# Optimization experiments

Measured on AMD Instinct MI355X. Metric: run time of the kernel, lower is better.

The kernel has to match this reference:

```python
import jax, jax.numpy as jnp
import numpy as np

L = 8          # number of QTT cores = log2(init_reso)
RESO = 256     # init_reso
MAX_RANK = 256
N_SAMPLES = 4096


def _qtt_ranks(L, max_rank):
    return [min(8 ** k, 8 ** (L - k), max_rank) for k in range(L + 1)]


def setup_inputs() -> dict:
    key = jax.random.key(0)
    ranks = _qtt_ranks(L, MAX_RANK)
    keys = jax.random.split(key, L + 1)
    inp = {}
    for l in range(L):
        shape = (ranks[l], 8, ranks[l + 1])
        scale = (shape[0] * shape[1]) ** -0.5  # keep chain products O(1)
        inp[f"core{l}"] = jax.random.normal(keys[l], shape, dtype=jnp.float32) * scale
    inp["coords_xyz"] = jax.random.randint(keys[L], (N_SAMPLES, 3), 0, RESO)
    return inp


def _coords_to_qtt(coords_xyz, num_cores):
    # coords_xyz: (N, 3) int. Per core l (most-significant bit first):
    # c_l = 4*bit_x + 2*bit_y + bit_z in [0, 8)  -> shape (L, N)
    x, y, z = coords_xyz[:, 0], coords_xyz[:, 1], coords_xyz[:, 2]
    shifts = jnp.arange(num_cores - 1, -1, -1)[:, None]  # (L, 1)
    bx = (x[None, :] >> shifts) & 1
    by = (y[None, :] >> shifts) & 1
    bz = (z[None, :] >> shifts) & 1
    return 4 * bx + 2 * by + bz


def _sample_tt(cores, coords):
    # cores[l]: (r_l, 8, r_{l+1}); coords: (L, N)
    # v starts as first core slice: (N, r_1)  (r_0 == 1)
    v = cores[0][0, coords[0], :]
    for l in range(1, len(cores)):
        # gathered slice: (r_l, N, r_{l+1}) -> (N, r_l, r_{l+1})
        g = jnp.transpose(cores[l][:, coords[l], :], (1, 0, 2))
        v = jnp.einsum('nr,nrs->ns', v, g)
    return v[:, 0]  # r_L == 1 -> (N,)


def reference(core0, core1, core2, core3, core4, core5, core6, core7, coords_xyz):
    cores = [core0, core1, core2, core3, core4, core5, core6, core7]
    coords = _coords_to_qtt(coords_xyz, len(cores))
    return _sample_tt(cores, coords)
```

## Files before the change

kernel.cpp:

```cpp
#include <hip/hip_runtime.h>


typedef unsigned int u32;

__device__ __forceinline__ void async_load16(const float* g, float* l) {
    __builtin_amdgcn_global_load_lds(
        (const __attribute__((address_space(1))) u32*)g,
        (__attribute__((address_space(3))) u32*)l, 16, 0, 0);
}
__device__ __forceinline__ void fma4(float4& c, float a, const float4& b) {
    c.x = fmaf(a, b.x, c.x); c.y = fmaf(a, b.y, c.y);
    c.z = fmaf(a, b.z, c.z); c.w = fmaf(a, b.w, c.w);
}
__device__ __forceinline__ int digit_of(int x, int y, int z, int sh) {
    return 4*((x>>sh)&1) + 2*((y>>sh)&1) + ((z>>sh)&1);
}

__global__ __launch_bounds__(256, 4) void tables_kernel(
    const float* __restrict__ C0, const float* __restrict__ C1,
    const float* __restrict__ C2, const float* __restrict__ C3,
    const float* __restrict__ C5, const float* __restrict__ C6,
    const float* __restrict__ C7,
    const int* __restrict__ coords, int n,
    int* __restrict__ perms, int* __restrict__ bases,
    float* __restrict__ P3, float* __restrict__ T)
{
    __shared__ __align__(16) union {
        struct { unsigned char digs[8192]; int cnt[8]; int offs[8]; } p;
        struct { float S6s[8][64]; } b;
        struct { float v64[8][64]; float As[8][260]; float Bs[2][16][256]; } g;
    } u;
    const int t = threadIdx.x;
    const int ln = t & 63, wv = t >> 6;
    const int bx = blockIdx.x;

    if (bx == 0) {
        if (t < 8) u.p.cnt[t] = 0;
        __syncthreads();
        for (int i = t; i < n; i += 256) {
            const int d = digit_of(coords[3*i], coords[3*i+1], coords[3*i+2], 3);
            u.p.digs[i] = (unsigned char)d;
            atomicAdd(&u.p.cnt[d], 1);
        }
        __syncthreads();
        if (t == 0) {
            int run = 0;
            for (int d = 0; d < 8; ++d) {
                u.p.offs[d] = run;
                bases[d] = run;
                run += u.p.cnt[d];
            }
            bases[8] = run;
        }
        __syncthreads();
        for (int i = t; i < n; i += 256) {
            const int pos = atomicAdd(&u.p.offs[u.p.digs[i]], 1);
            perms[pos] = i;
        }
    } else if (bx < 65) {
        const int bb = bx - 1;
        const int d5 = bb >> 3, d6 = bb & 7;
#pragma unroll
        for (int j = 0; j < 2; ++j) {
            const int idx = t + 256*j, d7 = idx >> 6, s = idx & 63;
            float acc = 0.f;
#pragma unroll
            for (int jj = 0; jj < 8; ++jj)
                acc = fmaf(C6[s*64 + d6*8 + jj], C7[jj*8 + d7], acc);
            u.b.S6s[d7][s] = acc;
        }
        __syncthreads();
        float4 creg[16];
#pragma unroll
        for (int s4 = 0; s4 < 16; ++s4)
            creg[s4] = *(const float4*)(C5 + (size_t)t*512 + d5*64 + s4*4);
#pragma unroll 1
        for (int d7 = 0; d7 < 8; ++d7) {
            float acc = 0.f;
#pragma unroll
            for (int s4 = 0; s4 < 16; ++s4) {
                const float4 a = creg[s4];
                const float4 b = *(const float4*)&u.b.S6s[d7][s4*4];
                acc = fmaf(a.x, b.x, acc); acc = fmaf(a.y, b.y, acc);
                acc = fmaf(a.z, b.z, acc); acc = fmaf(a.w, b.w, acc);
            }
            T[(size_t)((d5*8 + d6)*8 + d7)*256 + t] = acc;
        }
    } else {
        const int bb = bx - 65;
        const int d3 = bb & 7, d2 = (bb >> 3) & 7, d0 = bb >> 6;
        const float* Cd = C3 + d3 * 256;

        for (int r = wv; r < 16; r += 4)
            async_load16(Cd + (size_t)r*2048 + ln*4, &u.g.Bs[0][r][ln*4]);

#pragma unroll
        for (int j = 0; j < 2; ++j) {
            const int idx = t + 256*j, d1 = idx >> 6, c = idx & 63;
            float acc = 0.f;
#pragma unroll
            for (int r = 0; r < 8; ++r)
                acc = fmaf(C0[d0*8 + r], C1[r*512 + d1*64 + c], acc);
            u.g.v64[d1][c] = acc;
        }
        __syncthreads();

        {
            float4 accA0 = make_float4(0,0,0,0), accA1 = make_float4(0,0,0,0);
#pragma unroll 8
            for (int j = 0; j < 64; ++j) {
                const float4 c2 = *(const float4*)(C2 + (size_t)j*2048 + d2*256 + ln*4);
                fma4(accA0, u.g.v64[wv*2 + 0][j], c2);
                fma4(accA1, u.g.v64[wv*2 + 1][j], c2);
            }
            *(float4*)&u.g.As[wv*2 + 0][ln*4] = accA0;
            *(float4*)&u.g.As[wv*2 + 1][ln*4] = accA1;
        }
        __syncthreads();

        float4 acc0 = make_float4(0,0,0,0), acc1 = make_float4(0,0,0,0);
        for (int c = 0; c < 16; ++c) {
            if (c + 1 < 16) {
                const int nb = (c+1) & 1;
                for (int r = wv; r < 16; r += 4)
                    async_load16(Cd + (size_t)((c+1)*16 + r)*2048 + ln*4,
                                 &u.g.Bs[nb][r][ln*4]);
            }
            const int cb = c & 1, kb = c * 16;
#pragma unroll 1
            for (int k4 = 0; k4 < 16; k4 += 4) {
                const float4 a0 = *(const float4*)&u.g.As[wv*2 + 0][kb + k4];
                const float4 a1 = *(const float4*)&u.g.As[wv*2 + 1][kb + k4];
                const float4 b0v = *(const float4*)&u.g.Bs[cb][k4+0][ln*4];
                const float4 b1v = *(const float4*)&u.g.Bs[cb][k4+1][ln*4];
                const float4 b2v = *(const float4*)&u.g.Bs[cb][k4+2][ln*4];
                const float4 b3v = *(const float4*)&u.g.Bs[cb][k4+3][ln*4];
                fma4(acc0, a0.x, b0v); fma4(acc0, a0.y, b1v);
                fma4(acc0, a0.z, b2v); fma4(acc0, a0.w, b3v);
                fma4(acc1, a1.x, b0v); fma4(acc1, a1.y, b1v);
                fma4(acc1, a1.z, b2v); fma4(acc1, a1.w, b3v);
            }
            __syncthreads();
        }
        {
            const int a0i = d0*512 + (wv*2 + 0)*64 + d2*8 + d3;
            const int a1i = d0*512 + (wv*2 + 1)*64 + d2*8 + d3;
            *(float4*)(P3 + (size_t)a0i*256 + ln*4) = acc0;
            *(float4*)(P3 + (size_t)a1i*256 + ln*4) = acc1;
        }
    }
}

__global__ __launch_bounds__(256, 4) void stage4_final_kernel(
    const float* __restrict__ P3, const float* __restrict__ C4,
    const float* __restrict__ T, const int* __restrict__ coords,
    const int* __restrict__ perm, const int* __restrict__ base,
    float* __restrict__ out)
{
    const int d = blockIdx.x;
    const int b0 = base[d], b1 = base[d + 1];
    const int nrows = b1 - b0;
    const int t = threadIdx.x, ln = t & 63, wv = t >> 6;

    __shared__ __align__(16) float Arm[8][260];
    __shared__ __align__(16) float Bs[2][16][256];
    __shared__ int rows[8], aidx[8], qs[8];

    const float* Cd = C4 + d * 256;

    for (int tile = blockIdx.y; tile * 8 < nrows; tile += (int)gridDim.y) {
        const int row0 = b0 + tile * 8;

        for (int r = wv; r < 16; r += 4)
            async_load16(Cd + (size_t)r*2048 + ln*4, &Bs[0][r][ln*4]);
        if (t < 8) {
            const int gr = row0 + t;
            const int rr = (gr < b1) ? perm[gr] : -1;
            rows[t] = rr;
            int a = 0, q = 0;
            if (rr >= 0) {
                const int x = coords[3*rr], y = coords[3*rr+1], z = coords[3*rr+2];
                a = digit_of(x,y,z,7)*512 + digit_of(x,y,z,6)*64
                  + digit_of(x,y,z,5)*8 + digit_of(x,y,z,4);
                q = digit_of(x,y,z,2)*64 + digit_of(x,y,z,1)*8 + digit_of(x,y,z,0);
            }
            aidx[t] = a; qs[t] = q;
        }
        __syncthreads();

#pragma unroll
        for (int j = 0; j < 2; ++j) {
            const int idx = t + 256*j, s = idx >> 6, c4 = idx & 63;
            float4 v = make_float4(0,0,0,0);
            if (rows[s] >= 0)
                v = *(const float4*)(P3 + (size_t)aidx[s]*256 + c4*4);
            *(float4*)&Arm[s][c4*4] = v;
        }
        __syncthreads();

        float4 acc0 = make_float4(0,0,0,0), acc1 = make_float4(0,0,0,0);

        for (int c = 0; c < 16; ++c) {
            if (c + 1 < 16) {
                const int nb = (c+1) & 1;
                for (int r = wv; r < 16; r += 4)
                    async_load16(Cd + (size_t)((c+1)*16 + r)*2048 + ln*4,
                                 &Bs[nb][r][ln*4]);
            }
            const int cb = c & 1, kb = c * 16;
#pragma unroll 1
            for (int k4 = 0; k4 < 16; k4 += 4) {
                const float4 a0 = *(const float4*)&Arm[wv*2 + 0][kb + k4];
                const float4 a1 = *(const float4*)&Arm[wv*2 + 1][kb + k4];
                const float4 b0v = *(const float4*)&Bs[cb][k4+0][ln*4];
                const float4 b1v = *(const float4*)&Bs[cb][k4+1][ln*4];
                const float4 b2v = *(const float4*)&Bs[cb][k4+2][ln*4];
                const float4 b3v = *(const float4*)&Bs[cb][k4+3][ln*4];
                fma4(acc0, a0.x, b0v); fma4(acc0, a0.y, b1v);
                fma4(acc0, a0.z, b2v); fma4(acc0, a0.w, b3v);
                fma4(acc1, a1.x, b0v); fma4(acc1, a1.y, b1v);
                fma4(acc1, a1.z, b2v); fma4(acc1, a1.w, b3v);
            }
            __syncthreads();
        }

#pragma unroll
        for (int i = 0; i < 2; ++i) {
            const int s = wv*2 + i;
            const int rr = rows[s];
            float p = 0.f;
            if (rr >= 0) {
                const float4 a = (i == 0) ? acc0 : acc1;
                const float4 tv = *(const float4*)(T + (size_t)qs[s]*256 + ln*4);
                p = fmaf(a.x, tv.x, fmaf(a.y, tv.y, fmaf(a.z, tv.z, a.w * tv.w)));
            }
            p += __shfl_xor(p, 1);
            p += __shfl_xor(p, 2);
            p += __shfl_xor(p, 4);
            p += __shfl_xor(p, 8);
            p += __shfl_xor(p, 16);
            p += __shfl_xor(p, 32);
            if (ln == 0 && rr >= 0) out[rr] = p;
        }
        __syncthreads();
    }
}

extern "C" void kernel_launch(void* const* d_in, const int* in_sizes, int n_in,
                              void* d_out, int out_size, void* d_ws, size_t ws_size,
                              hipStream_t stream) {
    const float* C0 = (const float*)d_in[0];
    const float* C1 = (const float*)d_in[1];
    const float* C2 = (const float*)d_in[2];
    const float* C3 = (const float*)d_in[3];
    const float* C4 = (const float*)d_in[4];
    const float* C5 = (const float*)d_in[5];
    const float* C6 = (const float*)d_in[6];
    const float* C7 = (const float*)d_in[7];
    const int* coords = (const int*)d_in[8];
    float* out = (float*)d_out;

    const int n = in_sizes[8] / 3;

    float* P3   = (float*)d_ws;
    float* Tt   = P3 + 4096*256;
    int*   perms = (int*)(Tt + 512*256);
    int*   bases = perms + (size_t)n;

    tables_kernel<<<577, 256, 0, stream>>>(
        C0, C1, C2, C3, C5, C6, C7, coords, n, perms, bases, P3, Tt);
    stage4_final_kernel<<<dim3(8, 64), 256, 0, stream>>>(
        P3, C4, Tt, coords, perms, bases, out);
}
```

Measured before the change: 125.5 us.

## Split K across waves in GEMM loops to remove per-chunk block barriers

```diff
diff --git a/kernel.cpp b/kernel.cpp
--- a/kernel.cpp
+++ b/kernel.cpp
@@ -16,7 +16,7 @@
     return 4*((x>>sh)&1) + 2*((y>>sh)&1) + ((z>>sh)&1);
 }
 
-__global__ __launch_bounds__(256, 4) void tables_kernel(
+__global__ __launch_bounds__(256, 3) void tables_kernel(
     const float* __restrict__ C0, const float* __restrict__ C1,
     const float* __restrict__ C2, const float* __restrict__ C3,
     const float* __restrict__ C5, const float* __restrict__ C6,
@@ -28,7 +28,7 @@
     __shared__ __align__(16) union {
         struct { unsigned char digs[8192]; int cnt[8]; int offs[8]; } p;
         struct { float S6s[8][64]; } b;
-        struct { float v64[8][64]; float As[8][260]; float Bs[2][16][256]; } g;
+        struct { float v64[8][64]; float As[8][260]; float Bs[4][2][4][256]; } g;
     } u;
     const int t = threadIdx.x;
     const int ln = t & 63, wv = t >> 6;
@@ -90,9 +90,13 @@
         const int bb = bx - 65;
         const int d3 = bb & 7, d2 = (bb >> 3) & 7, d0 = bb >> 6;
         const float* Cd = C3 + d3 * 256;
-
-        for (int r = wv; r < 16; r += 4)
-            async_load16(Cd + (size_t)r*2048 + ln*4, &u.g.Bs[0][r][ln*4]);
+        float* BsF = &u.g.Bs[0][0][0][0];
+        const int kbase = wv * 64;
+
+#pragma unroll
+        for (int j = 0; j < 4; ++j)
+            async_load16(Cd + (size_t)(kbase + j)*2048 + ln*4,
+                         &u.g.Bs[wv][0][j][ln*4]);
 
 #pragma unroll
         for (int j = 0; j < 2; ++j) {
@@ -118,40 +122,60 @@
         }
         __syncthreads();
 
-        float4 acc0 = make_float4(0,0,0,0), acc1 = make_float4(0,0,0,0);
-        for (int c = 0; c < 16; ++c) {
-            if (c + 1 < 16) {
-                const int nb = (c+1) & 1;
-                for (int r = wv; r < 16; r += 4)
-                    async_load16(Cd + (size_t)((c+1)*16 + r)*2048 + ln*4,
-                                 &u.g.Bs[nb][r][ln*4]);
-            }
-            const int cb = c & 1, kb = c * 16;
+        float4 acc[8];
+#pragma unroll
+        for (int r = 0; r < 8; ++r) acc[r] = make_float4(0,0,0,0);
+
 #pragma unroll 1
-            for (int k4 = 0; k4 < 16; k4 += 4) {
-                const float4 a0 = *(const float4*)&u.g.As[wv*2 + 0][kb + k4];
-                const float4 a1 = *(const float4*)&u.g.As[wv*2 + 1][kb + k4];
-                const float4 b0v = *(const float4*)&u.g.Bs[cb][k4+0][ln*4];
-                const float4 b1v = *(const float4*)&u.g.Bs[cb][k4+1][ln*4];
-                const float4 b2v = *(const float4*)&u.g.Bs[cb][k4+2][ln*4];
-                const float4 b3v = *(const float4*)&u.g.Bs[cb][k4+3][ln*4];
-                fma4(acc0, a0.x, b0v); fma4(acc0, a0.y, b1v);
-                fma4(acc0, a0.z, b2v); fma4(acc0, a0.w, b3v);
-                fma4(acc1, a1.x, b0v); fma4(acc1, a1.y, b1v);
-                fma4(acc1, a1.z, b2v); fma4(acc1, a1.w, b3v);
-            }
-            __syncthreads();
-        }
+        for (int s = 0; s < 16; ++s) {
+            if (s < 15) {
+                const int nb = (s + 1) & 1;
+                const int ko = kbase + (s + 1) * 4;
+#pragma unroll
+                for (int j = 0; j < 4; ++j)
+                    async_load16(Cd + (size_t)(ko + j)*2048 + ln*4,
+                                 &u.g.Bs[wv][nb][j][ln*4]);
+                asm volatile("s_waitcnt vmcnt(4)" ::: "memory");
+            } else {
+                asm volatile("s_waitcnt vmcnt(0)" ::: "memory");
+            }
+            __builtin_amdgcn_sched_barrier(0);
+            const int cb = s & 1, kb = kbase + s * 4;
+            const float4 b0v = *(const float4*)&u.g.Bs[wv][cb][0][ln*4];
+            const float4 b1v = *(const float4*)&u.g.Bs[wv][cb][1][ln*4];
+            const float4 b2v = *(const float4*)&u.g.Bs[wv][cb][2][ln*4];
+            const float4 b3v = *(const float4*)&u.g.Bs[wv][cb][3][ln*4];
+#pragma unroll
+            for (int r = 0; r < 8; ++r) {
+                const float4 a = *(const float4*)&u.g.As[r][kb];
+                fma4(acc[r], a.x, b0v); fma4(acc[r], a.y, b1v);
+                fma4(acc[r], a.z, b2v); fma4(acc[r], a.w, b3v);
+            }
+        }
+
         {
-            const int a0i = d0*512 + (wv*2 + 0)*64 + d2*8 + d3;
-            const int a1i = d0*512 + (wv*2 + 1)*64 + d2*8 + d3;
-            *(float4*)(P3 + (size_t)a0i*256 + ln*4) = acc0;
-            *(float4*)(P3 + (size_t)a1i*256 + ln*4) = acc1;
+            float* my = BsF + wv * 2048;
+#pragma unroll
+            for (int r = 0; r < 8; ++r)
+                *(float4*)&my[r*256 + ln*4] = acc[r];
+        }
+        __syncthreads();
+#pragma unroll
+        for (int i = 0; i < 2; ++i) {
+            const int r = wv*2 + i;
+            float4 v = *(const float4*)&BsF[       r*256 + ln*4];
+            const float4 p1 = *(const float4*)&BsF[2048 + r*256 + ln*4];
+            const float4 p2 = *(const float4*)&BsF[4096 + r*256 + ln*4];
+            const float4 p3 = *(const float4*)&BsF[6144 + r*256 + ln*4];
+            v.x += p1.x + p2.x + p3.x; v.y += p1.y + p2.y + p3.y;
+            v.z += p1.z + p2.z + p3.z; v.w += p1.w + p2.w + p3.w;
+            const int ai = d0*512 + r*64 + d2*8 + d3;
+            *(float4*)(P3 + (size_t)ai*256 + ln*4) = v;
         }
     }
 }
 
-__global__ __launch_bounds__(256, 4) void stage4_final_kernel(
+__global__ __launch_bounds__(256, 2) void stage4_final_kernel(
     const float* __restrict__ P3, const float* __restrict__ C4,
     const float* __restrict__ T, const int* __restrict__ coords,
     const int* __restrict__ perm, const int* __restrict__ base,
@@ -163,16 +187,21 @@
     const int t = threadIdx.x, ln = t & 63, wv = t >> 6;
 
     __shared__ __align__(16) float Arm[8][260];
-    __shared__ __align__(16) float Bs[2][16][256];
+    __shared__ __align__(16) float Bs[4][2][4][256];
     __shared__ int rows[8], aidx[8], qs[8];
+    float* BsF = &Bs[0][0][0][0];
 
     const float* Cd = C4 + d * 256;
+    const int kbase = wv * 64;
 
     for (int tile = blockIdx.y; tile * 8 < nrows; tile += (int)gridDim.y) {
         const int row0 = b0 + tile * 8;
 
-        for (int r = wv; r < 16; r += 4)
-            async_load16(Cd + (size_t)r*2048 + ln*4, &Bs[0][r][ln*4]);
+#pragma unroll
+        for (int j = 0; j < 4; ++j)
+            async_load16(Cd + (size_t)(kbase + j)*2048 + ln*4,
+                         &Bs[wv][0][j][ln*4]);
+
         if (t < 8) {
             const int gr = row0 + t;
             const int rr = (gr < b1) ? perm[gr] : -1;
@@ -198,41 +227,59 @@
         }
         __syncthreads();
 
-        float4 acc0 = make_float4(0,0,0,0), acc1 = make_float4(0,0,0,0);
-
-        for (int c = 0; c < 16; ++c) {
-            if (c + 1 < 16) {
-                const int nb = (c+1) & 1;
-                for (int r = wv; r < 16; r += 4)
-                    async_load16(Cd + (size_t)((c+1)*16 + r)*2048 + ln*4,
-                                 &Bs[nb][r][ln*4]);
-            }
-            const int cb = c & 1, kb = c * 16;
+        float4 acc[8];
+#pragma unroll
+        for (int r = 0; r < 8; ++r) acc[r] = make_float4(0,0,0,0);
+
 #pragma unroll 1
-            for (int k4 = 0; k4 < 16; k4 += 4) {
-                const float4 a0 = *(const float4*)&Arm[wv*2 + 0][kb + k4];
-                const float4 a1 = *(const float4*)&Arm[wv*2 + 1][kb + k4];
-                const float4 b0v = *(const float4*)&Bs[cb][k4+0][ln*4];
-                const float4 b1v = *(const float4*)&Bs[cb][k4+1][ln*4];
-                const float4 b2v = *(const float4*)&Bs[cb][k4+2][ln*4];
-                const float4 b3v = *(const float4*)&Bs[cb][k4+3][ln*4];
-                fma4(acc0, a0.x, b0v); fma4(acc0, a0.y, b1v);
-                fma4(acc0, a0.z, b2v); fma4(acc0, a0.w, b3v);
-                fma4(acc1, a1.x, b0v); fma4(acc1, a1.y, b1v);
-                fma4(acc1, a1.z, b2v); fma4(acc1, a1.w, b3v);
-            }
-            __syncthreads();
-        }
+        for (int s = 0; s < 16; ++s) {
+            if (s < 15) {
+                const int nb = (s + 1) & 1;
+                const int ko = kbase + (s + 1) * 4;
+#pragma unroll
+                for (int j = 0; j < 4; ++j)
+                    async_load16(Cd + (size_t)(ko + j)*2048 + ln*4,
+                                 &Bs[wv][nb][j][ln*4]);
+                asm volatile("s_waitcnt vmcnt(4)" ::: "memory");
+            } else {
+                asm volatile("s_waitcnt vmcnt(0)" ::: "memory");
+            }
+            __builtin_amdgcn_sched_barrier(0);
+            const int cb = s & 1, kb = kbase + s * 4;
+            const float4 b0v = *(const float4*)&Bs[wv][cb][0][ln*4];
+            const float4 b1v = *(const float4*)&Bs[wv][cb][1][ln*4];
+            const float4 b2v = *(const float4*)&Bs[wv][cb][2][ln*4];
+            const float4 b3v = *(const float4*)&Bs[wv][cb][3][ln*4];
+#pragma unroll
+            for (int r = 0; r < 8; ++r) {
+                const float4 a = *(const float4*)&Arm[r][kb];
+                fma4(acc[r], a.x, b0v); fma4(acc[r], a.y, b1v);
+                fma4(acc[r], a.z, b2v); fma4(acc[r], a.w, b3v);
+            }
+        }
+
+        {
+            float* my = BsF + wv * 2048;
+#pragma unroll
+            for (int r = 0; r < 8; ++r)
+                *(float4*)&my[r*256 + ln*4] = acc[r];
+        }
+        __syncthreads();
 
 #pragma unroll
         for (int i = 0; i < 2; ++i) {
-            const int s = wv*2 + i;
-            const int rr = rows[s];
+            const int r = wv*2 + i;
+            const int rr = rows[r];
             float p = 0.f;
             if (rr >= 0) {
-                const float4 a = (i == 0) ? acc0 : acc1;
-                const float4 tv = *(const float4*)(T + (size_t)qs[s]*256 + ln*4);
-                p = fmaf(a.x, tv.x, fmaf(a.y, tv.y, fmaf(a.z, tv.z, a.w * tv.w)));
+                float4 v = *(const float4*)&BsF[       r*256 + ln*4];
+                const float4 p1 = *(const float4*)&BsF[2048 + r*256 + ln*4];
+                const float4 p2 = *(const float4*)&BsF[4096 + r*256 + ln*4];
+                const float4 p3 = *(const float4*)&BsF[6144 + r*256 + ln*4];
+                v.x += p1.x + p2.x + p3.x; v.y += p1.y + p2.y + p3.y;
+                v.z += p1.z + p2.z + p3.z; v.w += p1.w + p2.w + p3.w;
+                const float4 tv = *(const float4*)(T + (size_t)qs[r]*256 + ln*4);
+                p = fmaf(v.x, tv.x, fmaf(v.y, tv.y, fmaf(v.z, tv.z, v.w * tv.w)));
             }
             p += __shfl_xor(p, 1);
             p += __shfl_xor(p, 2);
```

Result: faster. 115.3 us (-8.2%).
